# Kernel optimization log

Measured on AMD Instinct MI355X. Metric: run time of the kernel, lower is better.

Reference implementation:

```python
import jax, jax.numpy as jnp
import numpy as np

NUM_HEADS = 4
HEAD_DIM = 64
BN_EPS = 1e-5

def _leaky_relu(x, slope=0.2):
    return jnp.where(x >= 0, x, slope * x)

def _gat_conv(x, W, a_src, a_dst, src, dst):
    # x: [N, F_in], W: [F_out, F_in], a_*: [H, D]; edges src/dst: [E]
    N = x.shape[0]
    h = (x @ W.T).reshape(N, NUM_HEADS, HEAD_DIM)          # [N, H, D]
    s_src = jnp.einsum('nhd,hd->nh', h, a_src)              # [N, H]
    s_dst = jnp.einsum('nhd,hd->nh', h, a_dst)              # [N, H]
    e = _leaky_relu(s_src[src] + s_dst[dst])                # [E, H]
    # segment softmax over edges grouped by dst; torch index_reduce_ starts
    # from zeros (include_self=True) -> max with 0
    e_max = jnp.maximum(jax.ops.segment_max(e, dst, num_segments=N), 0.0)
    e_exp = jnp.exp(e - e_max[dst])                         # [E, H]
    e_sum = jax.ops.segment_sum(e_exp, dst, num_segments=N) # [N, H]
    alpha = e_exp / jnp.maximum(e_sum[dst], 1e-9)           # [E, H]
    msg = h[src] * alpha[..., None]                         # [E, H, D]
    out = jax.ops.segment_sum(msg, dst, num_segments=N)     # [N, H, D]
    return out.reshape(N, NUM_HEADS * HEAD_DIM)

def _bn_eval(x, gamma, beta, mean, var):
    return (x - mean) * jax.lax.rsqrt(var + BN_EPS) * gamma + beta

def _elu(x):
    return jnp.where(x > 0, x, jnp.expm1(x))

def setup_inputs() -> dict:
    key = jax.random.key(0)
    ks = jax.random.split(key, 12)
    N, E, IN, HID, OUT = 50000, 500000, 256, 256, 64
    s = 0.05
    return {
        'x': jax.random.normal(ks[0], (N, IN), jnp.float32),
        'edge_index': jax.random.randint(ks[1], (2, E), 0, N, jnp.int64),
        'W1': jax.random.normal(ks[2], (HID, IN), jnp.float32) * s,
        'a_src1': jax.random.normal(ks[3], (NUM_HEADS, HEAD_DIM), jnp.float32) * s,
        'a_dst1': jax.random.normal(ks[4], (NUM_HEADS, HEAD_DIM), jnp.float32) * s,
        'bn1_gamma': jnp.ones((HID,), jnp.float32),
        'bn1_beta': jnp.zeros((HID,), jnp.float32),
        'bn1_mean': jnp.zeros((HID,), jnp.float32),
        'bn1_var': jnp.ones((HID,), jnp.float32),
        'W2': jax.random.normal(ks[5], (HID, HID), jnp.float32) * s,
        'a_src2': jax.random.normal(ks[6], (NUM_HEADS, HEAD_DIM), jnp.float32) * s,
        'a_dst2': jax.random.normal(ks[7], (NUM_HEADS, HEAD_DIM), jnp.float32) * s,
        'bn2_gamma': jnp.ones((HID,), jnp.float32),
        'bn2_beta': jnp.zeros((HID,), jnp.float32),
        'bn2_mean': jnp.zeros((HID,), jnp.float32),
        'bn2_var': jnp.ones((HID,), jnp.float32),
        'Wc': jax.random.normal(ks[8], (OUT, HID), jnp.float32) * s,
        'bc': jnp.zeros((OUT,), jnp.float32),
    }

def reference(x, edge_index, W1, a_src1, a_dst1, bn1_gamma, bn1_beta, bn1_mean, bn1_var,
              W2, a_src2, a_dst2, bn2_gamma, bn2_beta, bn2_mean, bn2_var, Wc, bc):
    src, dst = edge_index[0], edge_index[1]
    h = _gat_conv(x, W1, a_src1, a_dst1, src, dst)
    h = _elu(_bn_eval(h, bn1_gamma, bn1_beta, bn1_mean, bn1_var))
    h = _gat_conv(h, W2, a_src2, a_dst2, src, dst)
    h = _elu(_bn_eval(h, bn2_gamma, bn2_beta, bn2_mean, bn2_var))
    return h @ Wc.T + bc
```

## Files before the change

kernel.cpp:

```cpp
#include <hip/hip_runtime.h>

typedef __attribute__((ext_vector_type(8))) short short8;
typedef __attribute__((ext_vector_type(4))) float f32x4;

#define FF 256
#define NHEAD 4
#define HDIM 64
#define LDS_PITCH 264
#define BUCKET_CAP 64

__device__ __forceinline__ float bf2f(unsigned short u) {
  union { unsigned u; float f; } v; v.u = ((unsigned)u) << 16; return v.f;
}
__device__ __forceinline__ unsigned short f2bf(float f) {
  union { unsigned u; float f; } v; v.f = f;
  unsigned r = v.u + 0x7FFFu + ((v.u >> 16) & 1u);
  return (unsigned short)(r >> 16);
}

__device__ __forceinline__ short8 loadA8(const unsigned short* p) {
  return *(const short8*)p;
}
__device__ __forceinline__ short8 loadA8(const float* p) {
  f32x4 a = *(const f32x4*)p;
  f32x4 b = *(const f32x4*)(p + 4);
  short8 r;
  r[0] = (short)f2bf(a.x); r[1] = (short)f2bf(a.y);
  r[2] = (short)f2bf(a.z); r[3] = (short)f2bf(a.w);
  r[4] = (short)f2bf(b.x); r[5] = (short)f2bf(b.y);
  r[6] = (short)f2bf(b.z); r[7] = (short)f2bf(b.w);
  return r;
}

__global__ __launch_bounds__(256) void cvtw_kernel(
    const float* __restrict__ p0, int n0, const float* __restrict__ p1, int n1,
    const float* __restrict__ p2, int n2,
    unsigned short* __restrict__ o0, unsigned short* __restrict__ o1,
    unsigned short* __restrict__ o2, int* __restrict__ deg, int nz4) {
  int i = blockIdx.x * 256 + threadIdx.x;
  if (i < n0 + n1) {
    const float* in = (i < n0) ? p0 : p1;
    unsigned short* out = (i < n0) ? o0 : o1;
    int idx = (i < n0) ? i : i - n0;
    f32x4 v = ((const f32x4*)in)[idx];
    ushort4 o;
    o.x = f2bf(v.x); o.y = f2bf(v.y); o.z = f2bf(v.z); o.w = f2bf(v.w);
    ((ushort4*)out)[idx] = o;
  } else if (i < n0 + n1 + n2) {
    int idx = i - n0 - n1;
    f32x4 v = ((const f32x4*)p2)[idx];
    int e = idx * 4;
    int c = e >> 8;
    int f = e & 255;
    unsigned u0 = (unsigned)f2bf(v.x) | ((unsigned)f2bf(v.y) << 16);
    unsigned u1 = (unsigned)f2bf(v.z) | ((unsigned)f2bf(v.w) << 16);
    unsigned* W32 = (unsigned*)o2;
    int pb = f >> 1;
    W32[(pb + 0) * 64 + c] = u0;
    W32[(pb + 1) * 64 + c] = u1;
  } else {
    int z = i - n0 - n1 - n2;
    if (z < nz4) ((int4*)deg)[z] = int4{0, 0, 0, 0};
  }
}

__global__ __launch_bounds__(256) void gemm1_scatter(
    const float* __restrict__ A, const unsigned short* __restrict__ B,
    unsigned short* __restrict__ Cb, const float* __restrict__ a_src,
    const float* __restrict__ a_dst, float* __restrict__ sS,
    float* __restrict__ sD, int M, int gemmBlocks,
    const int* __restrict__ src, const int* __restrict__ dst,
    int* __restrict__ deg, int* __restrict__ bucket, int E) {
  const int K = 256;
  int tid = threadIdx.x;

  if (blockIdx.x >= gemmBlocks) {
    int i = (blockIdx.x - gemmBlocks) * 256 + tid;
    if (i < E) {
      int d = dst[i];
      int s = src[i];
      if ((unsigned)d < (unsigned)M) {
        int p = atomicAdd(&deg[d], 1);
        if (p < BUCKET_CAP)
          bucket[(size_t)d * BUCKET_CAP + p] = ((unsigned)s < (unsigned)M) ? s : 0;
      }
    }
    return;
  }

  __shared__ unsigned short Atile[64 * LDS_PITCH];
  int wave = tid >> 6;
  int lane = tid & 63;
  int row0w = blockIdx.x * 64;
  int col0 = wave * 64;
  int lr = lane & 15;
  int quad = lane >> 4;

  short8 breg[4][8];
  {
    const unsigned short* Bp0 = B + (size_t)(col0 + lr) * K + quad * 8;
#pragma unroll
    for (int t = 0; t < 4; ++t)
#pragma unroll
      for (int kk = 0; kk < 8; ++kk)
        breg[t][kk] = *(const short8*)(Bp0 + (size_t)(16 * t) * K + kk * 32);
  }

  {
#pragma unroll
    for (int pass = 0; pass < 8; ++pass) {
      int c = tid + pass * 256;
      int row = c >> 5;
      int col8 = (c & 31) * 8;
      int grow = row0w + row;
      if (grow >= M) grow = M - 1;
      short8 v = loadA8(A + (size_t)grow * K + col8);
      *(short8*)(&Atile[row * LDS_PITCH + col8]) = v;
    }
  }
  __syncthreads();

  f32x4 acc[4][4];
#pragma unroll
  for (int rt = 0; rt < 4; ++rt)
#pragma unroll
    for (int t = 0; t < 4; ++t) acc[rt][t] = f32x4{0, 0, 0, 0};

#pragma unroll
  for (int kk = 0; kk < 8; ++kk) {
    short8 a[4];
#pragma unroll
    for (int rt = 0; rt < 4; ++rt)
      a[rt] = *(const short8*)(&Atile[(rt * 16 + lr) * LDS_PITCH + quad * 8 + kk * 32]);
#pragma unroll
    for (int rt = 0; rt < 4; ++rt)
#pragma unroll
      for (int t = 0; t < 4; ++t)
        acc[rt][t] = __builtin_amdgcn_mfma_f32_16x16x32_bf16(a[rt], breg[t][kk], acc[rt][t], 0, 0, 0);
  }

#pragma unroll
  for (int rt = 0; rt < 4; ++rt) {
#pragma unroll
    for (int t = 0; t < 4; ++t) {
#pragma unroll
      for (int r = 0; r < 4; ++r) {
        int row = row0w + rt * 16 + quad * 4 + r;
        if (row < M) {
          int col = col0 + 16 * t + lr;
          Cb[(size_t)row * FF + col] = f2bf(acc[rt][t][r]);
        }
      }
    }
  }

  {
    float asv[4], adv[4];
#pragma unroll
    for (int t = 0; t < 4; ++t) {
      asv[t] = a_src[col0 + 16 * t + lr];
      adv[t] = a_dst[col0 + 16 * t + lr];
    }
#pragma unroll
    for (int rt = 0; rt < 4; ++rt) {
#pragma unroll
      for (int r = 0; r < 4; ++r) {
        float ps = acc[rt][0][r] * asv[0] + acc[rt][1][r] * asv[1] +
                   acc[rt][2][r] * asv[2] + acc[rt][3][r] * asv[3];
        float pd = acc[rt][0][r] * adv[0] + acc[rt][1][r] * adv[1] +
                   acc[rt][2][r] * adv[2] + acc[rt][3][r] * adv[3];
#pragma unroll
        for (int sft = 1; sft < 16; sft <<= 1) {
          ps += __shfl_xor(ps, sft);
          pd += __shfl_xor(pd, sft);
        }
        if (lr == 0) {
          int row = row0w + rt * 16 + quad * 4 + r;
          if (row < M) {
            sS[row * NHEAD + wave] = ps;
            sD[row * NHEAD + wave] = pd;
          }
        }
      }
    }
  }
}

__global__ __launch_bounds__(256) void gemm_main(const unsigned short* __restrict__ A,
                                                 const unsigned short* __restrict__ B,
                                                 unsigned short* __restrict__ Cb,
                                                 const float* __restrict__ a_src,
                                                 const float* __restrict__ a_dst,
                                                 float* __restrict__ sS,
                                                 float* __restrict__ sD,
                                                 int M) {
  __shared__ unsigned short Atile[64 * LDS_PITCH];
  const int K = 256;
  int tid = threadIdx.x;
  int wave = tid >> 6;
  int lane = tid & 63;
  int row0w = blockIdx.x * 64;
  int col0 = wave * 64;
  int lr = lane & 15;
  int quad = lane >> 4;

  short8 breg[4][8];
  {
    const unsigned short* Bp0 = B + (size_t)(col0 + lr) * K + quad * 8;
#pragma unroll
    for (int t = 0; t < 4; ++t)
#pragma unroll
      for (int kk = 0; kk < 8; ++kk)
        breg[t][kk] = *(const short8*)(Bp0 + (size_t)(16 * t) * K + kk * 32);
  }

  {
#pragma unroll
    for (int pass = 0; pass < 8; ++pass) {
      int c = tid + pass * 256;
      int row = c >> 5;
      int col8 = (c & 31) * 8;
      int grow = row0w + row;
      if (grow >= M) grow = M - 1;
      short8 v = loadA8(A + (size_t)grow * K + col8);
      *(short8*)(&Atile[row * LDS_PITCH + col8]) = v;
    }
  }
  __syncthreads();

  f32x4 acc[4][4];
#pragma unroll
  for (int rt = 0; rt < 4; ++rt)
#pragma unroll
    for (int t = 0; t < 4; ++t) acc[rt][t] = f32x4{0, 0, 0, 0};

#pragma unroll
  for (int kk = 0; kk < 8; ++kk) {
    short8 a[4];
#pragma unroll
    for (int rt = 0; rt < 4; ++rt)
      a[rt] = *(const short8*)(&Atile[(rt * 16 + lr) * LDS_PITCH + quad * 8 + kk * 32]);
#pragma unroll
    for (int rt = 0; rt < 4; ++rt)
#pragma unroll
      for (int t = 0; t < 4; ++t)
        acc[rt][t] = __builtin_amdgcn_mfma_f32_16x16x32_bf16(a[rt], breg[t][kk], acc[rt][t], 0, 0, 0);
  }

#pragma unroll
  for (int rt = 0; rt < 4; ++rt) {
#pragma unroll
    for (int t = 0; t < 4; ++t) {
#pragma unroll
      for (int r = 0; r < 4; ++r) {
        int row = row0w + rt * 16 + quad * 4 + r;
        if (row < M) {
          int col = col0 + 16 * t + lr;
          Cb[(size_t)row * FF + col] = f2bf(acc[rt][t][r]);
        }
      }
    }
  }

  {
    float asv[4], adv[4];
#pragma unroll
    for (int t = 0; t < 4; ++t) {
      asv[t] = a_src[col0 + 16 * t + lr];
      adv[t] = a_dst[col0 + 16 * t + lr];
    }
#pragma unroll
    for (int rt = 0; rt < 4; ++rt) {
#pragma unroll
      for (int r = 0; r < 4; ++r) {
        float ps = acc[rt][0][r] * asv[0] + acc[rt][1][r] * asv[1] +
                   acc[rt][2][r] * asv[2] + acc[rt][3][r] * asv[3];
        float pd = acc[rt][0][r] * adv[0] + acc[rt][1][r] * adv[1] +
                   acc[rt][2][r] * adv[2] + acc[rt][3][r] * adv[3];
#pragma unroll
        for (int sft = 1; sft < 16; sft <<= 1) {
          ps += __shfl_xor(ps, sft);
          pd += __shfl_xor(pd, sft);
        }
        if (lr == 0) {
          int row = row0w + rt * 16 + quad * 4 + r;
          if (row < M) {
            sS[row * NHEAD + wave] = ps;
            sD[row * NHEAD + wave] = pd;
          }
        }
      }
    }
  }
}

template <bool WITH_HEAD>
__global__ __launch_bounds__(256) void aggregate_kernel(
    const unsigned short* __restrict__ hprev, const float* __restrict__ sS,
    const float* __restrict__ sD, const int* __restrict__ deg,
    const int* __restrict__ bucket, const float* __restrict__ gamma,
    const float* __restrict__ beta, const float* __restrict__ mean,
    const float* __restrict__ var, unsigned short* __restrict__ hout,
    const unsigned short* __restrict__ wcT, const float* __restrict__ bc,
    float* __restrict__ outF, int N) {
  extern __shared__ char smem[];
  unsigned* wcs = (unsigned*)smem;
  float* hrow = (float*)(smem + 32768);

  int tid = threadIdx.x;
  int wave = tid >> 6;
  int lane = tid & 63;

  if constexpr (WITH_HEAD) {
    const unsigned* wsrc = (const unsigned*)wcT;
    for (int i = tid; i < 8192; i += 256) wcs[i] = wsrc[i];
    __syncthreads();
  }

  int n = blockIdx.x * 4 + wave;
  bool active = (n < N);
  if constexpr (!WITH_HEAD) {
    if (!active) return;
  }
  int hh = lane >> 4;
  int slot = lane & 15;
  int f0 = lane * 4;
  int srcBase = lane & 48;
  int dg = active ? deg[n] : 0;
  if (dg > BUCKET_CAP) dg = BUCKET_CAP;
  int jb = n * BUCKET_CAP;
  int je = jb + dg;
  int jlast = je - 1;
  float sdv = active ? sD[n * NHEAD + hh] : 0.f;
  float l = 0.f;
  float o0 = 0.f, o1 = 0.f, o2 = 0.f, o3 = 0.f;

  for (int c = jb; c < je; c += 16) {
    int j = c + slot;
    int jc = (j < jlast) ? j : jlast;
    int s = bucket[jc];
    float e = sS[s * NHEAD + hh] + sdv;
    e = (e >= 0.f) ? e : 0.2f * e;
    float w = (j < je) ? __expf(e) : 0.f;
    l += w;

    {
      uint2 u[8];
#pragma unroll
      for (int k = 0; k < 8; ++k) {
        int sk = __shfl(s, srcBase + k, 64);
        u[k] = *(const uint2*)(hprev + (size_t)sk * FF + f0);
      }
#pragma unroll
      for (int k = 0; k < 8; ++k) {
        float a = __shfl(w, srcBase + k, 64);
        o0 += a * __uint_as_float(u[k].x << 16);
        o1 += a * __uint_as_float(u[k].x & 0xffff0000u);
        o2 += a * __uint_as_float(u[k].y << 16);
        o3 += a * __uint_as_float(u[k].y & 0xffff0000u);
      }
    }
    if (c + 8 < je) {
      uint2 u[8];
#pragma unroll
      for (int k = 8; k < 16; ++k) {
        int sk = __shfl(s, srcBase + k, 64);
        u[k - 8] = *(const uint2*)(hprev + (size_t)sk * FF + f0);
      }
#pragma unroll
      for (int k = 8; k < 16; ++k) {
        float a = __shfl(w, srcBase + k, 64);
        o0 += a * __uint_as_float(u[k - 8].x << 16);
        o1 += a * __uint_as_float(u[k - 8].x & 0xffff0000u);
        o2 += a * __uint_as_float(u[k - 8].y << 16);
        o3 += a * __uint_as_float(u[k - 8].y & 0xffff0000u);
      }
    }
  }

  l += __shfl_xor(l, 1);
  l += __shfl_xor(l, 2);
  l += __shfl_xor(l, 4);
  l += __shfl_xor(l, 8);
  float li = 1.f / fmaxf(l, 1e-9f);

  f32x4 g = *(const f32x4*)(gamma + f0);
  f32x4 b = *(const f32x4*)(beta + f0);
  f32x4 mu = *(const f32x4*)(mean + f0);
  f32x4 vr = *(const f32x4*)(var + f0);
  float v0 = (o0 * li - mu.x) * rsqrtf(vr.x + 1e-5f) * g.x + b.x;
  float v1 = (o1 * li - mu.y) * rsqrtf(vr.y + 1e-5f) * g.y + b.y;
  float v2 = (o2 * li - mu.z) * rsqrtf(vr.z + 1e-5f) * g.z + b.z;
  float v3 = (o3 * li - mu.w) * rsqrtf(vr.w + 1e-5f) * g.w + b.w;
  v0 = (v0 > 0.f) ? v0 : expm1f(v0);
  v1 = (v1 > 0.f) ? v1 : expm1f(v1);
  v2 = (v2 > 0.f) ? v2 : expm1f(v2);
  v3 = (v3 > 0.f) ? v3 : expm1f(v3);

  if constexpr (!WITH_HEAD) {
    ushort4 ov;
    ov.x = f2bf(v0); ov.y = f2bf(v1); ov.z = f2bf(v2); ov.w = f2bf(v3);
    *(ushort4*)(hout + (size_t)n * FF + f0) = ov;
  } else {
    if (active)
      *(f32x4*)(&hrow[wave * 256 + f0]) = f32x4{v0, v1, v2, v3};
    __syncthreads();
    if (active) {
      const float* hr = &hrow[wave * 256];
      float acc = 0.f;
#pragma unroll 8
      for (int p4 = 0; p4 < 64; ++p4) {
        f32x4 h = *(const f32x4*)(hr + p4 * 4);
        unsigned wa = wcs[(2 * p4 + 0) * 64 + lane];
        unsigned wb = wcs[(2 * p4 + 1) * 64 + lane];
        acc += h.x * __uint_as_float(wa << 16);
        acc += h.y * __uint_as_float(wa & 0xffff0000u);
        acc += h.z * __uint_as_float(wb << 16);
        acc += h.w * __uint_as_float(wb & 0xffff0000u);
      }
      outF[(size_t)n * 64 + lane] = acc + bc[lane];
    }
  }
}

extern "C" void kernel_launch(void* const* d_in, const int* in_sizes, int n_in,
                              void* d_out, int out_size, void* d_ws, size_t ws_size,
                              hipStream_t stream) {
  const float* x   = (const float*)d_in[0];
  const int* ei    = (const int*)d_in[1];
  const float* W1  = (const float*)d_in[2];
  const float* as1 = (const float*)d_in[3];
  const float* ad1 = (const float*)d_in[4];
  const float* g1  = (const float*)d_in[5];
  const float* b1  = (const float*)d_in[6];
  const float* m1  = (const float*)d_in[7];
  const float* v1  = (const float*)d_in[8];
  const float* W2  = (const float*)d_in[9];
  const float* as2 = (const float*)d_in[10];
  const float* ad2 = (const float*)d_in[11];
  const float* g2  = (const float*)d_in[12];
  const float* b2  = (const float*)d_in[13];
  const float* m2  = (const float*)d_in[14];
  const float* v2  = (const float*)d_in[15];
  const float* Wc  = (const float*)d_in[16];
  const float* bc  = (const float*)d_in[17];

  const int N = in_sizes[0] / FF;
  const int E = in_sizes[1] / 2;
  const int* srcIdx = ei;
  const int* dstIdx = ei + E;

  char* ws = (char*)d_ws;
  size_t off = 0;
  auto take = [&](size_t bytes) -> void* {
    void* p = ws + off;
    off += (bytes + 255) & ~(size_t)255;
    return p;
  };
  const int N4 = (N + 3) & ~3;
  int* deg        = (int*)take((size_t)N4 * 4);
  int* bucket     = (int*)take((size_t)N * BUCKET_CAP * 4);
  float* sS       = (float*)take((size_t)N * NHEAD * 4);
  float* sD       = (float*)take((size_t)N * NHEAD * 4);
  unsigned short* hpre = (unsigned short*)take((size_t)N * FF * 2);
  unsigned short* hact = (unsigned short*)take((size_t)N * FF * 2);
  unsigned short* w1b  = (unsigned short*)take((size_t)FF * FF * 2);
  unsigned short* w2b  = (unsigned short*)take((size_t)FF * FF * 2);
  unsigned short* wcb  = (unsigned short*)take((size_t)64 * FF * 2);

  const int tpb = 256;

  {
    int n0 = (FF * FF) / 4, n1 = (FF * FF) / 4, n2 = (64 * FF) / 4;
    int nz4 = N4 / 4;
    int tot = n0 + n1 + n2 + nz4;
    cvtw_kernel<<<(tot + tpb - 1) / tpb, tpb, 0, stream>>>(W1, n0, W2, n1, Wc, n2,
                                                           w1b, w2b, wcb, deg, nz4);
  }

  int aggBlocks = (N + 3) / 4;
  int gemmBlocks = (N + 63) / 64;
  int scatBlocks = (E + tpb - 1) / tpb;

  gemm1_scatter<<<gemmBlocks + scatBlocks, 256, 0, stream>>>(
      x, w1b, hpre, as1, ad1, sS, sD, N, gemmBlocks, srcIdx, dstIdx, deg, bucket, E);
  aggregate_kernel<false><<<aggBlocks, 256, 0, stream>>>(
      hpre, sS, sD, deg, bucket, g1, b1, m1, v1, hact, wcb, bc, (float*)d_out, N);
  gemm_main<<<gemmBlocks, 256, 0, stream>>>(hact, w2b, hpre, as2, ad2, sS, sD, N);
  aggregate_kernel<true><<<aggBlocks, 256, 36864, stream>>>(
      hpre, sS, sD, deg, bucket, g2, b2, m2, v2, hact, wcb, bc, (float*)d_out, N);
}
```

Baseline: 342.0 us.

## Compute classifier head with MFMA in final aggregate, drop LDS weight staging

The final aggregate kernel no longer copies the transposed 32KB classifier weights into LDS per block or runs a per-lane scalar dot product over 256 features. It now packs the four node rows into a small zero-padded 16-row bf16 tile in static LDS and computes the 64-wide head with 16x16x32 bf16 MFMA, reading weights directly from global in row-major layout. The weight conversion kernel is simplified to a plain conversion without the transposed layout, and launch bounds request 8 blocks per CU. The intent is to cut per-block LDS fill traffic and raise occupancy. The cost is 12 of 16 MFMA rows wasted on padding and hidden-activation precision reduced to bf16 before the head.

```diff
diff --git a/kernel.cpp b/kernel.cpp
--- a/kernel.cpp
+++ b/kernel.cpp
@@ -38,30 +38,21 @@
     unsigned short* __restrict__ o0, unsigned short* __restrict__ o1,
     unsigned short* __restrict__ o2, int* __restrict__ deg, int nz4) {
   int i = blockIdx.x * 256 + threadIdx.x;
-  if (i < n0 + n1) {
-    const float* in = (i < n0) ? p0 : p1;
-    unsigned short* out = (i < n0) ? o0 : o1;
-    int idx = (i < n0) ? i : i - n0;
-    f32x4 v = ((const f32x4*)in)[idx];
-    ushort4 o;
-    o.x = f2bf(v.x); o.y = f2bf(v.y); o.z = f2bf(v.z); o.w = f2bf(v.w);
-    ((ushort4*)out)[idx] = o;
-  } else if (i < n0 + n1 + n2) {
-    int idx = i - n0 - n1;
-    f32x4 v = ((const f32x4*)p2)[idx];
-    int e = idx * 4;
-    int c = e >> 8;
-    int f = e & 255;
-    unsigned u0 = (unsigned)f2bf(v.x) | ((unsigned)f2bf(v.y) << 16);
-    unsigned u1 = (unsigned)f2bf(v.z) | ((unsigned)f2bf(v.w) << 16);
-    unsigned* W32 = (unsigned*)o2;
-    int pb = f >> 1;
-    W32[(pb + 0) * 64 + c] = u0;
-    W32[(pb + 1) * 64 + c] = u1;
-  } else {
+  const float* in;
+  unsigned short* out;
+  int idx;
+  if (i < n0) { in = p0; out = o0; idx = i; }
+  else if (i < n0 + n1) { in = p1; out = o1; idx = i - n0; }
+  else if (i < n0 + n1 + n2) { in = p2; out = o2; idx = i - n0 - n1; }
+  else {
     int z = i - n0 - n1 - n2;
     if (z < nz4) ((int4*)deg)[z] = int4{0, 0, 0, 0};
-  }
+    return;
+  }
+  f32x4 v = ((const f32x4*)in)[idx];
+  ushort4 o;
+  o.x = f2bf(v.x); o.y = f2bf(v.y); o.z = f2bf(v.z); o.w = f2bf(v.w);
+  ((ushort4*)out)[idx] = o;
 }
 
 __global__ __launch_bounds__(256) void gemm1_scatter(
@@ -295,28 +286,17 @@
 }
 
 template <bool WITH_HEAD>
-__global__ __launch_bounds__(256) void aggregate_kernel(
+__global__ __launch_bounds__(256, 8) void aggregate_kernel(
     const unsigned short* __restrict__ hprev, const float* __restrict__ sS,
     const float* __restrict__ sD, const int* __restrict__ deg,
     const int* __restrict__ bucket, const float* __restrict__ gamma,
     const float* __restrict__ beta, const float* __restrict__ mean,
     const float* __restrict__ var, unsigned short* __restrict__ hout,
-    const unsigned short* __restrict__ wcT, const float* __restrict__ bc,
+    const unsigned short* __restrict__ wc, const float* __restrict__ bc,
     float* __restrict__ outF, int N) {
-  extern __shared__ char smem[];
-  unsigned* wcs = (unsigned*)smem;
-  float* hrow = (float*)(smem + 32768);
-
   int tid = threadIdx.x;
   int wave = tid >> 6;
   int lane = tid & 63;
-
-  if constexpr (WITH_HEAD) {
-    const unsigned* wsrc = (const unsigned*)wcT;
-    for (int i = tid; i < 8192; i += 256) wcs[i] = wsrc[i];
-    __syncthreads();
-  }
-
   int n = blockIdx.x * 4 + wave;
   bool active = (n < N);
   if constexpr (!WITH_HEAD) {
@@ -402,23 +382,34 @@
     ov.x = f2bf(v0); ov.y = f2bf(v1); ov.z = f2bf(v2); ov.w = f2bf(v3);
     *(ushort4*)(hout + (size_t)n * FF + f0) = ov;
   } else {
-    if (active)
-      *(f32x4*)(&hrow[wave * 256 + f0]) = f32x4{v0, v1, v2, v3};
+    __shared__ unsigned short h4[16 * LDS_PITCH];
+    {
+      ushort4 z{0, 0, 0, 0};
+      for (int i = tid; i < (12 * LDS_PITCH) / 4; i += 256)
+        ((ushort4*)(h4 + 4 * LDS_PITCH))[i] = z;
+    }
+    if (active) {
+      ushort4 hv;
+      hv.x = f2bf(v0); hv.y = f2bf(v1); hv.z = f2bf(v2); hv.w = f2bf(v3);
+      *(ushort4*)(&h4[wave * LDS_PITCH + f0]) = hv;
+    }
     __syncthreads();
-    if (active) {
-      const float* hr = &hrow[wave * 256];
-      float acc = 0.f;
-#pragma unroll 8
-      for (int p4 = 0; p4 < 64; ++p4) {
-        f32x4 h = *(const f32x4*)(hr + p4 * 4);
-        unsigned wa = wcs[(2 * p4 + 0) * 64 + lane];
-        unsigned wb = wcs[(2 * p4 + 1) * 64 + lane];
-        acc += h.x * __uint_as_float(wa << 16);
-        acc += h.y * __uint_as_float(wa & 0xffff0000u);
-        acc += h.z * __uint_as_float(wb << 16);
-        acc += h.w * __uint_as_float(wb & 0xffff0000u);
-      }
-      outF[(size_t)n * 64 + lane] = acc + bc[lane];
+    const unsigned short* Bp = wc + (size_t)(16 * wave + slot) * 256 + hh * 8;
+    f32x4 acc = f32x4{0, 0, 0, 0};
+#pragma unroll
+    for (int kk = 0; kk < 8; ++kk) {
+      short8 af = *(const short8*)(&h4[slot * LDS_PITCH + hh * 8 + kk * 32]);
+      short8 bf = *(const short8*)(Bp + kk * 32);
+      acc = __builtin_amdgcn_mfma_f32_16x16x32_bf16(af, bf, acc, 0, 0, 0);
+    }
+    if (hh == 0) {
+      int colg = 16 * wave + slot;
+      float bias = bc[colg];
+#pragma unroll
+      for (int r = 0; r < 4; ++r) {
+        int nn = blockIdx.x * 4 + r;
+        if (nn < N) outF[(size_t)nn * 64 + colg] = acc[r] + bias;
+      }
     }
   }
 }
@@ -487,6 +478,6 @@
   aggregate_kernel<false><<<aggBlocks, 256, 0, stream>>>(
       hpre, sS, sD, deg, bucket, g1, b1, m1, v1, hact, wcb, bc, (float*)d_out, N);
   gemm_main<<<gemmBlocks, 256, 0, stream>>>(hact, w2b, hpre, as2, ad2, sS, sD, N);
-  aggregate_kernel<true><<<aggBlocks, 256, 36864, stream>>>(
+  aggregate_kernel<true><<<aggBlocks, 256, 0, stream>>>(
       hpre, sS, sD, deg, bucket, g2, b2, m2, v2, hact, wcb, bc, (float*)d_out, N);
 }
```

After: 318.6 us. 1.07x faster.
